# Kernel optimization log

Hardware: AMD Instinct MI355X
Metric: run time of the kernel (lower is better)

Reference implementation:

```python
import jax, jax.numpy as jnp
import numpy as np

H = 128        # hidden_dim
FEAT = 32      # feat_dim
LAYERS = 4     # 'layers' init arg -> residual MLP stacks of LAYERS+1 linears
M = 32768      # nodes per topological level
L = 16         # number of topological levels
MU = M // 2    # unary nodes per level (rest binary)
N = M * L      # total nodes


def setup_inputs() -> dict:
    key = jax.random.key(0)
    ks = jax.random.split(key, 10)

    def lin(k, out, inn):
        kw, kb = jax.random.split(k)
        s = 1.0 / np.sqrt(inn)
        return (jax.random.uniform(kw, (out, inn), minval=-s, maxval=s, dtype=jnp.float32),
                jax.random.uniform(kb, (out,), minval=-s, maxval=s, dtype=jnp.float32))

    def lin_stack(k, n, out, inn):
        kw, kb = jax.random.split(k)
        s = 1.0 / np.sqrt(inn)
        return (jax.random.uniform(kw, (n, out, inn), minval=-s, maxval=s, dtype=jnp.float32),
                jax.random.uniform(kb, (n, out), minval=-s, maxval=s, dtype=jnp.float32))

    emb_w, emb_b = lin(ks[0], H, FEAT)          # embed_op: feat_dim -> H
    ne0_w, ne0_b = lin(ks[1], H, 2 * H)         # node_embeds[0]: 2H -> H
    ne_w, ne_b = lin_stack(ks[2], LAYERS, H, H) # node_embeds[1..]: H -> H
    mpu_w, mpu_b = lin_stack(ks[3], LAYERS + 1, H, H)  # mp_unary: all H -> H
    mpb0_w, mpb0_b = lin(ks[4], H, 2 * H)       # mp_binary[0]: 2H -> H
    mpb_w, mpb_b = lin_stack(ks[5], LAYERS, H, H)      # mp_binary[1..]: H -> H

    node_feats = jax.random.normal(ks[6], (N, FEAT), dtype=jnp.float32)

    # Layered DAG: node at level l>=1 has two candidate parents in level l-1.
    pk = jax.random.split(ks[7], L)
    rows = [jnp.zeros((M, 2), dtype=jnp.int32)]  # level-0 rows unused
    for l in range(1, L):
        rows.append(jax.random.randint(pk[l], (M, 2), 0, M, dtype=jnp.int32) + (l - 1) * M)
    parents = jnp.concatenate(rows, 0)

    return dict(node_feats=node_feats, emb_w=emb_w, emb_b=emb_b,
                ne0_w=ne0_w, ne0_b=ne0_b, ne_w=ne_w, ne_b=ne_b,
                mpu_w=mpu_w, mpu_b=mpu_b, mpb0_w=mpb0_w, mpb0_b=mpb0_b,
                mpb_w=mpb_w, mpb_b=mpb_b, parents=parents)


def _stack_mlp(x, w0, b0, ws, bs):
    """relu(lay0) -> relu(lay1) -> residual relu layers: act(lay(a[-2]+a[-1]))."""
    a0 = jax.nn.relu(x @ w0.T + b0)
    a1 = jax.nn.relu(a0 @ ws[0].T + bs[0])
    p2, p1 = a0, a1
    for i in range(1, ws.shape[0]):
        cur = jax.nn.relu((p2 + p1) @ ws[i].T + bs[i])
        p2, p1 = p1, cur
    return p1


def reference(node_feats, emb_w, emb_b, ne0_w, ne0_b, ne_w, ne_b,
              mpu_w, mpu_b, mpb0_w, mpb0_b, mpb_w, mpb_b, parents):
    base = jax.nn.relu(node_feats @ emb_w.T + emb_b)  # [N, H] embed_op for all nodes
    E = jnp.zeros((N, H), dtype=base.dtype)
    E = E.at[:M].set(base[:M])  # roots: no messages -> embeds = relu(embed_op)
    for l in range(1, L):  # topological propagation, one level at a time
        s = l * M
        pl = parents[s:s + M]
        # unary nodes: gather one parent embedding, mp_unary stack
        msg_u = E[pl[:MU, 0]]                                  # [MU, H]
        redux_u = _stack_mlp(msg_u, mpu_w[0], mpu_b[0], mpu_w[1:], mpu_b[1:])
        # binary nodes: gather + concat two parent embeddings, mp_binary stack
        msg_b = E[pl[MU:]].reshape(M - MU, 2 * H)              # [MB, 2H]
        redux_b = _stack_mlp(msg_b, mpb0_w, mpb0_b, mpb_w, mpb_b)
        redux = jnp.concatenate([redux_u, redux_b], axis=0)    # [M, H]
        # apply_func: concat(embed, msgs_redux) -> node_embeds stack
        x = jnp.concatenate([base[s:s + M], redux], axis=-1)   # [M, 2H]
        E = E.at[s:s + M].set(_stack_mlp(x, ne0_w, ne0_b, ne_w, ne_b))
    return E
```

## Files before the change

kernel.cpp:

```cpp
#include <hip/hip_runtime.h>
#include <hip/hip_bf16.h>


#define H        128
#define FEAT     32
#define M_NODES  32768
#define L_LAYERS 16
#define MU_      (M_NODES / 2)
#define N_TOTAL  (M_NODES * L_LAYERS)

typedef __bf16 bf16x8 __attribute__((ext_vector_type(8)));
typedef __bf16 bf16x4 __attribute__((ext_vector_type(4)));
typedef float  f32x4  __attribute__((ext_vector_type(4)));

#define SLOT_MPU(l) ((l) * 32)
#define SLOT_MPB0   160
#define SLOT_MPB(l) (224 + (l) * 32)
#define SLOT_NE0    352
#define SLOT_NE(l)  (416 + (l) * 32)
#define TOTAL_FP    544

#define CG_SWZ(row, cg) ((cg) ^ ((row) & 7))

__global__ void prep_kernel(__bf16* __restrict__ frags,
                            const float* __restrict__ mpu_w,
                            const float* __restrict__ mpb0_w,
                            const float* __restrict__ mpb_w,
                            const float* __restrict__ ne0_w,
                            const float* __restrict__ ne_w) {
  int fp = blockIdx.x * 4 + (threadIdx.x >> 6);
  if (fp >= TOTAL_FP) return;
  int lane = threadIdx.x & 63;
  const float* src; int K; int idx;
  if (fp < 160)      { src = mpu_w + (fp >> 5) * H * H;         K = H;     idx = fp & 31; }
  else if (fp < 224) { src = mpb0_w;                            K = 2 * H; idx = fp - 160; }
  else if (fp < 352) { src = mpb_w + ((fp - 224) >> 5) * H * H; K = H;     idx = (fp - 224) & 31; }
  else if (fp < 416) { src = ne0_w;                             K = 2 * H; idx = fp - 352; }
  else               { src = ne_w + ((fp - 416) >> 5) * H * H;  K = H;     idx = (fp - 416) & 31; }
  int KT = K >> 5;
  int ct = idx / KT, kt = idx - ct * KT;
  int col = ct * 16 + (lane & 15);
  int k0  = kt * 32 + (lane >> 4) * 8;
  __bf16* dhi = frags + ((size_t)fp << 10) + lane * 8;
#pragma unroll
  for (int j = 0; j < 8; ++j) {
    float x  = src[col * K + k0 + j];
    __bf16 h = (__bf16)x;
    dhi[j]       = h;
    dhi[512 + j] = (__bf16)(x - (float)h);
  }
}

__global__ void embed_kernel(float* __restrict__ E,
                             const float* __restrict__ feats,
                             const float* __restrict__ emb_w,
                             const float* __restrict__ emb_b) {
  __shared__ float fl[64][36];
  int tid = threadIdx.x;
  size_t rbase = (size_t)blockIdx.x * 64;
  {
    int idx = tid;
#pragma unroll
    for (int rep = 0; rep < 2; ++rep, idx += 256) {
      int r = idx >> 3, c4 = idx & 7;
      *(f32x4*)&fl[r][c4 * 4] = *(const f32x4*)(feats + (rbase + r) * FEAT + c4 * 4);
    }
  }
  __syncthreads();
  int o = tid & 127, rh = tid >> 7;
  float w[32];
#pragma unroll
  for (int i = 0; i < 8; ++i) {
    f32x4 v = *(const f32x4*)(emb_w + o * FEAT + i * 4);
    w[i * 4 + 0] = v[0]; w[i * 4 + 1] = v[1]; w[i * 4 + 2] = v[2]; w[i * 4 + 3] = v[3];
  }
  float b = emb_b[o];
  for (int i = 0; i < 32; ++i) {
    int r = rh * 32 + i;
    float acc = b;
#pragma unroll
    for (int k4 = 0; k4 < 8; ++k4) {
      f32x4 f = *(const f32x4*)&fl[r][k4 * 4];
      acc += f[0] * w[k4 * 4] + f[1] * w[k4 * 4 + 1] + f[2] * w[k4 * 4 + 2] + f[3] * w[k4 * 4 + 3];
    }
    E[(rbase + r) * H + o] = fmaxf(acc, 0.f);
  }
}

struct Wkt { bf16x8 h[4]; bf16x8 l[4]; };

__device__ __forceinline__ void load_wkt(Wkt& w, const __bf16* __restrict__ frags,
                                         int slot, int KT, int kt, int wc, int lane) {
#pragma unroll
  for (int c = 0; c < 4; ++c) {
    const __bf16* fb =
        frags + (((size_t)(slot + (wc * 4 + c) * KT + kt)) << 10) + lane * 8;
    w.h[c] = *(const bf16x8*)fb;
    w.l[c] = *(const bf16x8*)(fb + 512);
  }
}

__device__ __forceinline__ void zero_acc(f32x4 (&acc)[2][4]) {
  f32x4 z = {0.f, 0.f, 0.f, 0.f};
#pragma unroll
  for (int i = 0; i < 2; ++i)
#pragma unroll
    for (int c = 0; c < 4; ++c) acc[i][c] = z;
}

__device__ __forceinline__ void gemm(f32x4 (&acc)[2][4],
                                     const __bf16* Ph, const __bf16* Pl,
                                     const __bf16* __restrict__ frags, int slot, int KT,
                                     int ktoff, int wr, int wc, int lane) {
  int r16 = lane & 15, g = lane >> 4;
  Wkt w0, w1;
  load_wkt(w0, frags, slot, KT, ktoff, wc, lane);
  bf16x8 ah[2][4], al[2][4];
#pragma unroll
  for (int i = 0; i < 2; ++i) {
    int row = wr * 32 + i * 16 + r16;
#pragma unroll
    for (int kt = 0; kt < 4; ++kt) {
      int off = row * H + CG_SWZ(row, kt * 4 + g) * 8;
      ah[i][kt] = *(const bf16x8*)(Ph + off);
      al[i][kt] = *(const bf16x8*)(Pl + off);
    }
  }
#pragma unroll
  for (int kt = 0; kt < 4; ++kt) {
    Wkt& cur = (kt & 1) ? w1 : w0;
    Wkt& nxt = (kt & 1) ? w0 : w1;
    if (kt < 3) load_wkt(nxt, frags, slot, KT, ktoff + kt + 1, wc, lane);
#pragma unroll
    for (int i = 0; i < 2; ++i)
#pragma unroll
      for (int c = 0; c < 4; ++c)
        acc[i][c] = __builtin_amdgcn_mfma_f32_16x16x32_bf16(cur.h[c], ah[i][kt], acc[i][c], 0, 0, 0);
#pragma unroll
    for (int i = 0; i < 2; ++i)
#pragma unroll
      for (int c = 0; c < 4; ++c)
        acc[i][c] = __builtin_amdgcn_mfma_f32_16x16x32_bf16(cur.l[c], ah[i][kt], acc[i][c], 0, 0, 0);
#pragma unroll
    for (int i = 0; i < 2; ++i)
#pragma unroll
      for (int c = 0; c < 4; ++c)
        acc[i][c] = __builtin_amdgcn_mfma_f32_16x16x32_bf16(cur.h[c], al[i][kt], acc[i][c], 0, 0, 0);
  }
}

__device__ __forceinline__ void epilogue(const f32x4 (&acc)[2][4], const float* __restrict__ bias,
                                         int mode, float* __restrict__ eout, int wr, int wc,
                                         int lane, __bf16* Ch, __bf16* Cl, __bf16* Sh, __bf16* Sl) {
  int r16 = lane & 15, g = lane >> 4;
#pragma unroll
  for (int c = 0; c < 4; ++c) {
    int c0 = wc * 64 + c * 16 + g * 4;
    f32x4 bv = *(const f32x4*)(bias + c0);
#pragma unroll
    for (int i = 0; i < 2; ++i) {
      int row = wr * 32 + i * 16 + r16;
      f32x4 v;
#pragma unroll
      for (int j = 0; j < 4; ++j) v[j] = fmaxf(acc[i][c][j] + bv[j], 0.f);
      if (mode == 2) {
        *(f32x4*)(eout + (size_t)row * H + c0) = v;
      } else {
        int off = row * H + CG_SWZ(row, c0 >> 3) * 8 + (c0 & 7);
        if (mode == 1) {
          bf16x4 oh = *(bf16x4*)(Ch + off), ol = *(bf16x4*)(Cl + off);
          bf16x4 sh, sl;
#pragma unroll
          for (int j = 0; j < 4; ++j) {
            float sv = v[j] + (float)oh[j] + (float)ol[j];
            __bf16 t = (__bf16)sv;
            sh[j] = t; sl[j] = (__bf16)(sv - (float)t);
          }
          *(bf16x4*)(Sh + off) = sh; *(bf16x4*)(Sl + off) = sl;
        }
        bf16x4 h, l;
#pragma unroll
        for (int j = 0; j < 4; ++j) {
          __bf16 t = (__bf16)v[j];
          h[j] = t; l[j] = (__bf16)(v[j] - (float)t);
        }
        *(bf16x4*)(Ch + off) = h; *(bf16x4*)(Cl + off) = l;
      }
    }
  }
}

__device__ __forceinline__ void stage_row(const float* __restrict__ src, __bf16* Ph, __bf16* Pl,
                                          int row, int q) {
#pragma unroll
  for (int i = 0; i < 4; ++i) {
    int cg = q * 4 + i;
    f32x4 f0 = *(const f32x4*)(src + cg * 8);
    f32x4 f1 = *(const f32x4*)(src + cg * 8 + 4);
    bf16x8 h, l;
#pragma unroll
    for (int j = 0; j < 4; ++j) {
      __bf16 t = (__bf16)f0[j]; h[j] = t; l[j] = (__bf16)(f0[j] - (float)t);
    }
#pragma unroll
    for (int j = 0; j < 4; ++j) {
      __bf16 t = (__bf16)f1[j]; h[4 + j] = t; l[4 + j] = (__bf16)(f1[j] - (float)t);
    }
    int off = row * H + CG_SWZ(row, cg) * 8;
    *(bf16x8*)(Ph + off) = h;
    *(bf16x8*)(Pl + off) = l;
  }
}

__global__ __launch_bounds__(256, 2) void phase_kernel(
    float* __restrict__ E, const int* __restrict__ parents, const __bf16* __restrict__ frags,
    const float* __restrict__ mpu_b, const float* __restrict__ mpb0_b,
    const float* __restrict__ mpb_b, const float* __restrict__ ne0_b,
    const float* __restrict__ ne_b, int s) {
  __shared__ __bf16 Ch[64 * H], Cl[64 * H], Sh[64 * H], Sl[64 * H];
  int t = blockIdx.x;
  bool un = t < (MU_ / 64);
  int row0 = t * 64;
  int tid = threadIdx.x;
  int lane = tid & 63, wave = tid >> 6;
  int wr = wave >> 1, wc = wave & 1;
  int srow = tid >> 2, q = tid & 3;
  int gr = s + row0 + srow;

  f32x4 acc[2][4];

  if (un) {
    stage_row(E + (size_t)parents[2 * gr] * H, Ch, Cl, srow, q);
    __syncthreads();
    zero_acc(acc); gemm(acc, Ch, Cl, frags, SLOT_MPU(0), 4, 0, wr, wc, lane); __syncthreads();
    epilogue(acc, mpu_b, 0, nullptr, wr, wc, lane, Ch, Cl, Sh, Sl); __syncthreads();
    zero_acc(acc); gemm(acc, Ch, Cl, frags, SLOT_MPU(1), 4, 0, wr, wc, lane); __syncthreads();
    epilogue(acc, mpu_b + H, 1, nullptr, wr, wc, lane, Ch, Cl, Sh, Sl); __syncthreads();
    zero_acc(acc); gemm(acc, Sh, Sl, frags, SLOT_MPU(2), 4, 0, wr, wc, lane); __syncthreads();
    epilogue(acc, mpu_b + 2 * H, 1, nullptr, wr, wc, lane, Ch, Cl, Sh, Sl); __syncthreads();
    zero_acc(acc); gemm(acc, Sh, Sl, frags, SLOT_MPU(3), 4, 0, wr, wc, lane); __syncthreads();
    epilogue(acc, mpu_b + 3 * H, 1, nullptr, wr, wc, lane, Ch, Cl, Sh, Sl); __syncthreads();
    zero_acc(acc); gemm(acc, Sh, Sl, frags, SLOT_MPU(4), 4, 0, wr, wc, lane); __syncthreads();
    epilogue(acc, mpu_b + 4 * H, 0, nullptr, wr, wc, lane, Ch, Cl, Sh, Sl);
  } else {
    stage_row(E + (size_t)parents[2 * gr] * H, Sh, Sl, srow, q);
    stage_row(E + (size_t)parents[2 * gr + 1] * H, Ch, Cl, srow, q);
    __syncthreads();
    zero_acc(acc);
    gemm(acc, Sh, Sl, frags, SLOT_MPB0, 8, 0, wr, wc, lane);
    gemm(acc, Ch, Cl, frags, SLOT_MPB0, 8, 4, wr, wc, lane);
    __syncthreads();
    epilogue(acc, mpb0_b, 0, nullptr, wr, wc, lane, Ch, Cl, Sh, Sl); __syncthreads();
    zero_acc(acc); gemm(acc, Ch, Cl, frags, SLOT_MPB(0), 4, 0, wr, wc, lane); __syncthreads();
    epilogue(acc, mpb_b, 1, nullptr, wr, wc, lane, Ch, Cl, Sh, Sl); __syncthreads();
    zero_acc(acc); gemm(acc, Sh, Sl, frags, SLOT_MPB(1), 4, 0, wr, wc, lane); __syncthreads();
    epilogue(acc, mpb_b + H, 1, nullptr, wr, wc, lane, Ch, Cl, Sh, Sl); __syncthreads();
    zero_acc(acc); gemm(acc, Sh, Sl, frags, SLOT_MPB(2), 4, 0, wr, wc, lane); __syncthreads();
    epilogue(acc, mpb_b + 2 * H, 1, nullptr, wr, wc, lane, Ch, Cl, Sh, Sl); __syncthreads();
    zero_acc(acc); gemm(acc, Sh, Sl, frags, SLOT_MPB(3), 4, 0, wr, wc, lane); __syncthreads();
    epilogue(acc, mpb_b + 3 * H, 0, nullptr, wr, wc, lane, Ch, Cl, Sh, Sl);
  }

  stage_row(E + (size_t)(s + row0 + srow) * H, Sh, Sl, srow, q);
  __syncthreads();

  zero_acc(acc);
  gemm(acc, Sh, Sl, frags, SLOT_NE0, 8, 0, wr, wc, lane);
  gemm(acc, Ch, Cl, frags, SLOT_NE0, 8, 4, wr, wc, lane);
  __syncthreads();
  epilogue(acc, ne0_b, 0, nullptr, wr, wc, lane, Ch, Cl, Sh, Sl); __syncthreads();
  zero_acc(acc); gemm(acc, Ch, Cl, frags, SLOT_NE(0), 4, 0, wr, wc, lane); __syncthreads();
  epilogue(acc, ne_b, 1, nullptr, wr, wc, lane, Ch, Cl, Sh, Sl); __syncthreads();
  zero_acc(acc); gemm(acc, Sh, Sl, frags, SLOT_NE(1), 4, 0, wr, wc, lane); __syncthreads();
  epilogue(acc, ne_b + H, 1, nullptr, wr, wc, lane, Ch, Cl, Sh, Sl); __syncthreads();
  zero_acc(acc); gemm(acc, Sh, Sl, frags, SLOT_NE(2), 4, 0, wr, wc, lane); __syncthreads();
  epilogue(acc, ne_b + 2 * H, 1, nullptr, wr, wc, lane, Ch, Cl, Sh, Sl); __syncthreads();
  zero_acc(acc); gemm(acc, Sh, Sl, frags, SLOT_NE(3), 4, 0, wr, wc, lane);
  epilogue(acc, ne_b + 3 * H, 2, E + (size_t)(s + row0) * H, wr, wc, lane, Ch, Cl, Sh, Sl);
}

extern "C" void kernel_launch(void* const* d_in, const int* in_sizes, int n_in,
                              void* d_out, int out_size, void* d_ws, size_t ws_size,
                              hipStream_t stream) {
  const float* node_feats = (const float*)d_in[0];
  const float* emb_w  = (const float*)d_in[1];
  const float* emb_b  = (const float*)d_in[2];
  const float* ne0_w  = (const float*)d_in[3];
  const float* ne0_b  = (const float*)d_in[4];
  const float* ne_w   = (const float*)d_in[5];
  const float* ne_b   = (const float*)d_in[6];
  const float* mpu_w  = (const float*)d_in[7];
  const float* mpu_b  = (const float*)d_in[8];
  const float* mpb0_w = (const float*)d_in[9];
  const float* mpb0_b = (const float*)d_in[10];
  const float* mpb_w  = (const float*)d_in[11];
  const float* mpb_b  = (const float*)d_in[12];
  const int*   parents = (const int*)d_in[13];
  float* E = (float*)d_out;
  __bf16* frags = (__bf16*)d_ws;

  prep_kernel<<<(TOTAL_FP + 3) / 4, 256, 0, stream>>>(frags, mpu_w, mpb0_w, mpb_w, ne0_w, ne_w);
  embed_kernel<<<N_TOTAL / 64, 256, 0, stream>>>(E, node_feats, emb_w, emb_b);
  for (int l = 1; l < L_LAYERS; ++l) {
    phase_kernel<<<M_NODES / 64, 256, 0, stream>>>(E, parents, frags, mpu_b, mpb0_b, mpb_b,
                                                   ne0_b, ne_b, l * M_NODES);
  }
}
```

Before: 1.160 ms.

## Keep MLP activations in registers per wave and fuse embed into phase kernel

Restructures the phase kernel so each wave owns 32 rows and feeds each layer's output accumulators straight into the next layer's MFMA input fragments in registers. This removes the shared-memory staging and the block-wide barriers between layers. The prep kernel now permutes the K ordering of the weight fragments so accumulator layout matches input fragment layout. The residual term is kept in per-wave shared scratch without syncs. The base embedding is computed on the fly with MFMA inside each phase rather than by a separate full-graph embed kernel, and only level 0 is embedded up front. In exchange, register pressure is higher, occupancy drops to one block per SM (launch bounds), and weight fragments are loaded from global memory more often.

```diff
diff --git a/kernel.cpp b/kernel.cpp
--- a/kernel.cpp
+++ b/kernel.cpp
@@ -7,22 +7,22 @@
 #define M_NODES  32768
 #define L_LAYERS 16
 #define MU_      (M_NODES / 2)
-#define N_TOTAL  (M_NODES * L_LAYERS)
 
 typedef __bf16 bf16x8 __attribute__((ext_vector_type(8)));
-typedef __bf16 bf16x4 __attribute__((ext_vector_type(4)));
 typedef float  f32x4  __attribute__((ext_vector_type(4)));
 
-#define SLOT_MPU(l) ((l) * 32)
-#define SLOT_MPB0   160
-#define SLOT_MPB(l) (224 + (l) * 32)
-#define SLOT_NE0    352
-#define SLOT_NE(l)  (416 + (l) * 32)
-#define TOTAL_FP    544
-
-#define CG_SWZ(row, cg) ((cg) ^ ((row) & 7))
+#define MFMA_BF16 __builtin_amdgcn_mfma_f32_16x16x32_bf16
+
+#define SLOT_EMB    0
+#define SLOT_MPU(l) (8 + (l) * 32)
+#define SLOT_MPB0   168
+#define SLOT_MPB(l) (232 + (l) * 32)
+#define SLOT_NE0    360
+#define SLOT_NE(l)  (424 + (l) * 32)
+#define TOTAL_FP    552
 
 __global__ void prep_kernel(__bf16* __restrict__ frags,
+                            const float* __restrict__ emb_w,
                             const float* __restrict__ mpu_w,
                             const float* __restrict__ mpb0_w,
                             const float* __restrict__ mpb_w,
@@ -31,252 +31,261 @@
   int fp = blockIdx.x * 4 + (threadIdx.x >> 6);
   if (fp >= TOTAL_FP) return;
   int lane = threadIdx.x & 63;
+  int r16 = lane & 15, g = lane >> 4;
   const float* src; int K; int idx;
-  if (fp < 160)      { src = mpu_w + (fp >> 5) * H * H;         K = H;     idx = fp & 31; }
-  else if (fp < 224) { src = mpb0_w;                            K = 2 * H; idx = fp - 160; }
-  else if (fp < 352) { src = mpb_w + ((fp - 224) >> 5) * H * H; K = H;     idx = (fp - 224) & 31; }
-  else if (fp < 416) { src = ne0_w;                             K = 2 * H; idx = fp - 352; }
-  else               { src = ne_w + ((fp - 416) >> 5) * H * H;  K = H;     idx = (fp - 416) & 31; }
+  if (fp < 8)        { src = emb_w;                             K = 32;  idx = fp; }
+  else if (fp < 168) { src = mpu_w + ((fp - 8) >> 5) * H * H;   K = 128; idx = (fp - 8) & 31; }
+  else if (fp < 232) { src = mpb0_w;                            K = 256; idx = fp - 168; }
+  else if (fp < 360) { src = mpb_w + ((fp - 232) >> 5) * H * H; K = 128; idx = (fp - 232) & 31; }
+  else if (fp < 424) { src = ne0_w;                             K = 256; idx = fp - 360; }
+  else               { src = ne_w + ((fp - 424) >> 5) * H * H;  K = 128; idx = (fp - 424) & 31; }
   int KT = K >> 5;
-  int ct = idx / KT, kt = idx - ct * KT;
-  int col = ct * 16 + (lane & 15);
-  int k0  = kt * 32 + (lane >> 4) * 8;
+  int c = idx / KT, kt = idx - c * KT;
+  int col = c * 16 + r16;
   __bf16* dhi = frags + ((size_t)fp << 10) + lane * 8;
 #pragma unroll
   for (int j = 0; j < 8; ++j) {
-    float x  = src[col * K + k0 + j];
+    int k = kt * 32 + ((j >> 2) * 16 + g * 4 + (j & 3));
+    float x  = src[col * K + k];
     __bf16 h = (__bf16)x;
     dhi[j]       = h;
     dhi[512 + j] = (__bf16)(x - (float)h);
   }
 }
 
-__global__ void embed_kernel(float* __restrict__ E,
-                             const float* __restrict__ feats,
-                             const float* __restrict__ emb_w,
-                             const float* __restrict__ emb_b) {
-  __shared__ float fl[64][36];
-  int tid = threadIdx.x;
-  size_t rbase = (size_t)blockIdx.x * 64;
-  {
-    int idx = tid;
-#pragma unroll
-    for (int rep = 0; rep < 2; ++rep, idx += 256) {
-      int r = idx >> 3, c4 = idx & 7;
-      *(f32x4*)&fl[r][c4 * 4] = *(const f32x4*)(feats + (rbase + r) * FEAT + c4 * 4);
-    }
-  }
-  __syncthreads();
-  int o = tid & 127, rh = tid >> 7;
-  float w[32];
-#pragma unroll
-  for (int i = 0; i < 8; ++i) {
-    f32x4 v = *(const f32x4*)(emb_w + o * FEAT + i * 4);
-    w[i * 4 + 0] = v[0]; w[i * 4 + 1] = v[1]; w[i * 4 + 2] = v[2]; w[i * 4 + 3] = v[3];
-  }
-  float b = emb_b[o];
-  for (int i = 0; i < 32; ++i) {
-    int r = rh * 32 + i;
-    float acc = b;
-#pragma unroll
-    for (int k4 = 0; k4 < 8; ++k4) {
-      f32x4 f = *(const f32x4*)&fl[r][k4 * 4];
-      acc += f[0] * w[k4 * 4] + f[1] * w[k4 * 4 + 1] + f[2] * w[k4 * 4 + 2] + f[3] * w[k4 * 4 + 3];
-    }
-    E[(rbase + r) * H + o] = fmaxf(acc, 0.f);
-  }
-}
-
-struct Wkt { bf16x8 h[4]; bf16x8 l[4]; };
-
-__device__ __forceinline__ void load_wkt(Wkt& w, const __bf16* __restrict__ frags,
-                                         int slot, int KT, int kt, int wc, int lane) {
-#pragma unroll
-  for (int c = 0; c < 4; ++c) {
-    const __bf16* fb =
-        frags + (((size_t)(slot + (wc * 4 + c) * KT + kt)) << 10) + lane * 8;
-    w.h[c] = *(const bf16x8*)fb;
-    w.l[c] = *(const bf16x8*)(fb + 512);
-  }
-}
-
-__device__ __forceinline__ void zero_acc(f32x4 (&acc)[2][4]) {
+__device__ __forceinline__ void split_pair(const f32x4& a, const f32x4& b,
+                                           bf16x8& h, bf16x8& l) {
+#pragma unroll
+  for (int j = 0; j < 4; ++j) {
+    __bf16 t = (__bf16)a[j]; h[j] = t;     l[j] = (__bf16)(a[j] - (float)t);
+    __bf16 u = (__bf16)b[j]; h[4 + j] = u; l[4 + j] = (__bf16)(b[j] - (float)u);
+  }
+}
+
+__device__ __forceinline__ void zero_acc8(f32x4 (&acc)[2][8]) {
   f32x4 z = {0.f, 0.f, 0.f, 0.f};
 #pragma unroll
   for (int i = 0; i < 2; ++i)
 #pragma unroll
-    for (int c = 0; c < 4; ++c) acc[i][c] = z;
-}
-
-__device__ __forceinline__ void gemm(f32x4 (&acc)[2][4],
-                                     const __bf16* Ph, const __bf16* Pl,
-                                     const __bf16* __restrict__ frags, int slot, int KT,
-                                     int ktoff, int wr, int wc, int lane) {
+    for (int c = 0; c < 8; ++c) acc[i][c] = z;
+}
+
+__device__ __forceinline__ void gather_frags128(bf16x8 (&xh)[2][4], bf16x8 (&xl)[2][4],
+                                                const float* __restrict__ s0,
+                                                const float* __restrict__ s1, int g) {
+#pragma unroll
+  for (int i = 0; i < 2; ++i) {
+    const float* src = i ? s1 : s0;
+#pragma unroll
+    for (int kt = 0; kt < 4; ++kt) {
+      f32x4 a = *(const f32x4*)(src + kt * 32 + g * 4);
+      f32x4 b = *(const f32x4*)(src + kt * 32 + 16 + g * 4);
+      split_pair(a, b, xh[i][kt], xl[i][kt]);
+    }
+  }
+}
+
+__device__ __forceinline__ void stage128(f32x4 (&acc)[2][8],
+                                         const bf16x8 (&xh)[2][4], const bf16x8 (&xl)[2][4],
+                                         const __bf16* __restrict__ frags,
+                                         int fp0, int KT, int kt0, int lane) {
+#pragma unroll
+  for (int cp = 0; cp < 4; ++cp) {
+    const int c0 = 2 * cp, c1 = 2 * cp + 1;
+#pragma unroll
+    for (int kt = 0; kt < 4; ++kt) {
+      const __bf16* f0 = frags + (((size_t)(fp0 + c0 * KT + kt0 + kt)) << 10) + lane * 8;
+      const __bf16* f1 = frags + (((size_t)(fp0 + c1 * KT + kt0 + kt)) << 10) + lane * 8;
+      bf16x8 w0h = *(const bf16x8*)f0;
+      bf16x8 w0l = *(const bf16x8*)(f0 + 512);
+      bf16x8 w1h = *(const bf16x8*)f1;
+      bf16x8 w1l = *(const bf16x8*)(f1 + 512);
+      acc[0][c0] = MFMA_BF16(w0h, xh[0][kt], acc[0][c0], 0, 0, 0);
+      acc[0][c1] = MFMA_BF16(w1h, xh[0][kt], acc[0][c1], 0, 0, 0);
+      acc[1][c0] = MFMA_BF16(w0h, xh[1][kt], acc[1][c0], 0, 0, 0);
+      acc[1][c1] = MFMA_BF16(w1h, xh[1][kt], acc[1][c1], 0, 0, 0);
+      acc[0][c0] = MFMA_BF16(w0l, xh[0][kt], acc[0][c0], 0, 0, 0);
+      acc[0][c1] = MFMA_BF16(w1l, xh[0][kt], acc[0][c1], 0, 0, 0);
+      acc[1][c0] = MFMA_BF16(w0l, xh[1][kt], acc[1][c0], 0, 0, 0);
+      acc[1][c1] = MFMA_BF16(w1l, xh[1][kt], acc[1][c1], 0, 0, 0);
+      acc[0][c0] = MFMA_BF16(w0h, xl[0][kt], acc[0][c0], 0, 0, 0);
+      acc[0][c1] = MFMA_BF16(w1h, xl[0][kt], acc[0][c1], 0, 0, 0);
+      acc[1][c0] = MFMA_BF16(w0h, xl[1][kt], acc[1][c0], 0, 0, 0);
+      acc[1][c1] = MFMA_BF16(w1h, xl[1][kt], acc[1][c1], 0, 0, 0);
+    }
+  }
+}
+
+__device__ __forceinline__ void stage32(f32x4 (&acc)[2][8],
+                                        const bf16x8 (&fh)[2], const bf16x8 (&fl)[2],
+                                        const __bf16* __restrict__ frags, int fp0, int lane) {
+#pragma unroll
+  for (int cp = 0; cp < 4; ++cp) {
+    const int c0 = 2 * cp, c1 = 2 * cp + 1;
+    const __bf16* f0 = frags + (((size_t)(fp0 + c0)) << 10) + lane * 8;
+    const __bf16* f1 = frags + (((size_t)(fp0 + c1)) << 10) + lane * 8;
+    bf16x8 w0h = *(const bf16x8*)f0;
+    bf16x8 w0l = *(const bf16x8*)(f0 + 512);
+    bf16x8 w1h = *(const bf16x8*)f1;
+    bf16x8 w1l = *(const bf16x8*)(f1 + 512);
+    acc[0][c0] = MFMA_BF16(w0h, fh[0], acc[0][c0], 0, 0, 0);
+    acc[0][c1] = MFMA_BF16(w1h, fh[0], acc[0][c1], 0, 0, 0);
+    acc[1][c0] = MFMA_BF16(w0h, fh[1], acc[1][c0], 0, 0, 0);
+    acc[1][c1] = MFMA_BF16(w1h, fh[1], acc[1][c1], 0, 0, 0);
+    acc[0][c0] = MFMA_BF16(w0l, fh[0], acc[0][c0], 0, 0, 0);
+    acc[0][c1] = MFMA_BF16(w1l, fh[0], acc[0][c1], 0, 0, 0);
+    acc[1][c0] = MFMA_BF16(w0l, fh[1], acc[1][c0], 0, 0, 0);
+    acc[1][c1] = MFMA_BF16(w1l, fh[1], acc[1][c1], 0, 0, 0);
+    acc[0][c0] = MFMA_BF16(w0h, fl[0], acc[0][c0], 0, 0, 0);
+    acc[0][c1] = MFMA_BF16(w1h, fl[0], acc[0][c1], 0, 0, 0);
+    acc[1][c0] = MFMA_BF16(w0h, fl[1], acc[1][c0], 0, 0, 0);
+    acc[1][c1] = MFMA_BF16(w1h, fl[1], acc[1][c1], 0, 0, 0);
+  }
+}
+
+template <int PM>
+__device__ __forceinline__ void epilogue_frags(const f32x4 (&acc)[2][8],
+                                               const float* __restrict__ bias,
+                                               float* pv, int g,
+                                               bf16x8 (&xh)[2][4], bf16x8 (&xl)[2][4]) {
+#pragma unroll
+  for (int i = 0; i < 2; ++i)
+#pragma unroll
+    for (int kt = 0; kt < 4; ++kt) {
+      f32x4 x0, x1;
+#pragma unroll
+      for (int hf = 0; hf < 2; ++hf) {
+        const int c = 2 * kt + hf;
+        f32x4 bv = *(const f32x4*)(bias + c * 16 + g * 4);
+        f32x4 a, x;
+#pragma unroll
+        for (int j = 0; j < 4; ++j) a[j] = fmaxf(acc[i][c][j] + bv[j], 0.f);
+        x = a;
+        if (PM == 1) {
+          f32x4 p = *(const f32x4*)(pv + (i * 8 + c) * 256);
+#pragma unroll
+          for (int j = 0; j < 4; ++j) x[j] = a[j] + p[j];
+        }
+        if (PM != 2) *(f32x4*)(pv + (i * 8 + c) * 256) = a;
+        if (hf == 0) x0 = x; else x1 = x;
+      }
+      split_pair(x0, x1, xh[i][kt], xl[i][kt]);
+    }
+}
+
+__device__ __forceinline__ void epilogue_store(const f32x4 (&acc)[2][8],
+                                               const float* __restrict__ bias,
+                                               float* __restrict__ out, int r16, int g) {
+#pragma unroll
+  for (int i = 0; i < 2; ++i)
+#pragma unroll
+    for (int c = 0; c < 8; ++c) {
+      f32x4 bv = *(const f32x4*)(bias + c * 16 + g * 4);
+      f32x4 v;
+#pragma unroll
+      for (int j = 0; j < 4; ++j) v[j] = fmaxf(acc[i][c][j] + bv[j], 0.f);
+      *(f32x4*)(out + (size_t)(i * 16 + r16) * H + c * 16 + g * 4) = v;
+    }
+}
+
+__device__ __forceinline__ void feats_frags(bf16x8 (&fh)[2], bf16x8 (&fl)[2],
+                                            const float* __restrict__ feats,
+                                            int row_a, int row_b, int g) {
+#pragma unroll
+  for (int i = 0; i < 2; ++i) {
+    const float* src = feats + (size_t)(i ? row_b : row_a) * FEAT;
+    f32x4 a = *(const f32x4*)(src + g * 4);
+    f32x4 b = *(const f32x4*)(src + 16 + g * 4);
+    split_pair(a, b, fh[i], fl[i]);
+  }
+}
+
+__global__ __launch_bounds__(256, 1) void base0_kernel(float* __restrict__ E,
+                                                       const float* __restrict__ feats,
+                                                       const __bf16* __restrict__ frags,
+                                                       const float* __restrict__ emb_b) {
+  int tid = threadIdx.x, lane = tid & 63, wave = tid >> 6;
   int r16 = lane & 15, g = lane >> 4;
-  Wkt w0, w1;
-  load_wkt(w0, frags, slot, KT, ktoff, wc, lane);
-  bf16x8 ah[2][4], al[2][4];
-#pragma unroll
-  for (int i = 0; i < 2; ++i) {
-    int row = wr * 32 + i * 16 + r16;
-#pragma unroll
-    for (int kt = 0; kt < 4; ++kt) {
-      int off = row * H + CG_SWZ(row, kt * 4 + g) * 8;
-      ah[i][kt] = *(const bf16x8*)(Ph + off);
-      al[i][kt] = *(const bf16x8*)(Pl + off);
-    }
-  }
-#pragma unroll
-  for (int kt = 0; kt < 4; ++kt) {
-    Wkt& cur = (kt & 1) ? w1 : w0;
-    Wkt& nxt = (kt & 1) ? w0 : w1;
-    if (kt < 3) load_wkt(nxt, frags, slot, KT, ktoff + kt + 1, wc, lane);
-#pragma unroll
-    for (int i = 0; i < 2; ++i)
-#pragma unroll
-      for (int c = 0; c < 4; ++c)
-        acc[i][c] = __builtin_amdgcn_mfma_f32_16x16x32_bf16(cur.h[c], ah[i][kt], acc[i][c], 0, 0, 0);
-#pragma unroll
-    for (int i = 0; i < 2; ++i)
-#pragma unroll
-      for (int c = 0; c < 4; ++c)
-        acc[i][c] = __builtin_amdgcn_mfma_f32_16x16x32_bf16(cur.l[c], ah[i][kt], acc[i][c], 0, 0, 0);
-#pragma unroll
-    for (int i = 0; i < 2; ++i)
-#pragma unroll
-      for (int c = 0; c < 4; ++c)
-        acc[i][c] = __builtin_amdgcn_mfma_f32_16x16x32_bf16(cur.h[c], al[i][kt], acc[i][c], 0, 0, 0);
-  }
-}
-
-__device__ __forceinline__ void epilogue(const f32x4 (&acc)[2][4], const float* __restrict__ bias,
-                                         int mode, float* __restrict__ eout, int wr, int wc,
-                                         int lane, __bf16* Ch, __bf16* Cl, __bf16* Sh, __bf16* Sl) {
-  int r16 = lane & 15, g = lane >> 4;
-#pragma unroll
-  for (int c = 0; c < 4; ++c) {
-    int c0 = wc * 64 + c * 16 + g * 4;
-    f32x4 bv = *(const f32x4*)(bias + c0);
-#pragma unroll
-    for (int i = 0; i < 2; ++i) {
-      int row = wr * 32 + i * 16 + r16;
-      f32x4 v;
-#pragma unroll
-      for (int j = 0; j < 4; ++j) v[j] = fmaxf(acc[i][c][j] + bv[j], 0.f);
-      if (mode == 2) {
-        *(f32x4*)(eout + (size_t)row * H + c0) = v;
-      } else {
-        int off = row * H + CG_SWZ(row, c0 >> 3) * 8 + (c0 & 7);
-        if (mode == 1) {
-          bf16x4 oh = *(bf16x4*)(Ch + off), ol = *(bf16x4*)(Cl + off);
-          bf16x4 sh, sl;
-#pragma unroll
-          for (int j = 0; j < 4; ++j) {
-            float sv = v[j] + (float)oh[j] + (float)ol[j];
-            __bf16 t = (__bf16)sv;
-            sh[j] = t; sl[j] = (__bf16)(sv - (float)t);
-          }
-          *(bf16x4*)(Sh + off) = sh; *(bf16x4*)(Sl + off) = sl;
-        }
-        bf16x4 h, l;
-#pragma unroll
-        for (int j = 0; j < 4; ++j) {
-          __bf16 t = (__bf16)v[j];
-          h[j] = t; l[j] = (__bf16)(v[j] - (float)t);
-        }
-        *(bf16x4*)(Ch + off) = h; *(bf16x4*)(Cl + off) = l;
-      }
-    }
-  }
-}
-
-__device__ __forceinline__ void stage_row(const float* __restrict__ src, __bf16* Ph, __bf16* Pl,
-                                          int row, int q) {
-#pragma unroll
-  for (int i = 0; i < 4; ++i) {
-    int cg = q * 4 + i;
-    f32x4 f0 = *(const f32x4*)(src + cg * 8);
-    f32x4 f1 = *(const f32x4*)(src + cg * 8 + 4);
-    bf16x8 h, l;
-#pragma unroll
-    for (int j = 0; j < 4; ++j) {
-      __bf16 t = (__bf16)f0[j]; h[j] = t; l[j] = (__bf16)(f0[j] - (float)t);
-    }
-#pragma unroll
-    for (int j = 0; j < 4; ++j) {
-      __bf16 t = (__bf16)f1[j]; h[4 + j] = t; l[4 + j] = (__bf16)(f1[j] - (float)t);
-    }
-    int off = row * H + CG_SWZ(row, cg) * 8;
-    *(bf16x8*)(Ph + off) = h;
-    *(bf16x8*)(Pl + off) = l;
-  }
-}
-
-__global__ __launch_bounds__(256, 2) void phase_kernel(
-    float* __restrict__ E, const int* __restrict__ parents, const __bf16* __restrict__ frags,
+  int R0 = blockIdx.x * 128 + wave * 32;
+  bf16x8 fh[2], fl[2];
+  feats_frags(fh, fl, feats, R0 + r16, R0 + 16 + r16, g);
+  f32x4 acc[2][8];
+  zero_acc8(acc);
+  stage32(acc, fh, fl, frags, SLOT_EMB, lane);
+  epilogue_store(acc, emb_b, E + (size_t)R0 * H, r16, g);
+}
+
+__global__ __launch_bounds__(256, 1) void phase_kernel(
+    float* __restrict__ E, const int* __restrict__ parents,
+    const __bf16* __restrict__ frags, const float* __restrict__ feats,
+    const float* __restrict__ emb_b,
     const float* __restrict__ mpu_b, const float* __restrict__ mpb0_b,
     const float* __restrict__ mpb_b, const float* __restrict__ ne0_b,
     const float* __restrict__ ne_b, int s) {
-  __shared__ __bf16 Ch[64 * H], Cl[64 * H], Sh[64 * H], Sl[64 * H];
-  int t = blockIdx.x;
-  bool un = t < (MU_ / 64);
-  int row0 = t * 64;
-  int tid = threadIdx.x;
-  int lane = tid & 63, wave = tid >> 6;
-  int wr = wave >> 1, wc = wave & 1;
-  int srow = tid >> 2, q = tid & 3;
-  int gr = s + row0 + srow;
-
-  f32x4 acc[2][4];
-
-  if (un) {
-    stage_row(E + (size_t)parents[2 * gr] * H, Ch, Cl, srow, q);
-    __syncthreads();
-    zero_acc(acc); gemm(acc, Ch, Cl, frags, SLOT_MPU(0), 4, 0, wr, wc, lane); __syncthreads();
-    epilogue(acc, mpu_b, 0, nullptr, wr, wc, lane, Ch, Cl, Sh, Sl); __syncthreads();
-    zero_acc(acc); gemm(acc, Ch, Cl, frags, SLOT_MPU(1), 4, 0, wr, wc, lane); __syncthreads();
-    epilogue(acc, mpu_b + H, 1, nullptr, wr, wc, lane, Ch, Cl, Sh, Sl); __syncthreads();
-    zero_acc(acc); gemm(acc, Sh, Sl, frags, SLOT_MPU(2), 4, 0, wr, wc, lane); __syncthreads();
-    epilogue(acc, mpu_b + 2 * H, 1, nullptr, wr, wc, lane, Ch, Cl, Sh, Sl); __syncthreads();
-    zero_acc(acc); gemm(acc, Sh, Sl, frags, SLOT_MPU(3), 4, 0, wr, wc, lane); __syncthreads();
-    epilogue(acc, mpu_b + 3 * H, 1, nullptr, wr, wc, lane, Ch, Cl, Sh, Sl); __syncthreads();
-    zero_acc(acc); gemm(acc, Sh, Sl, frags, SLOT_MPU(4), 4, 0, wr, wc, lane); __syncthreads();
-    epilogue(acc, mpu_b + 4 * H, 0, nullptr, wr, wc, lane, Ch, Cl, Sh, Sl);
+  __shared__ float prevb[4 * 4096];
+  int tid = threadIdx.x, lane = tid & 63, wave = tid >> 6;
+  int r16 = lane & 15, g = lane >> 4;
+  int R0 = blockIdx.x * 128 + wave * 32;
+  float* pv = prevb + wave * 4096 + lane * 4;
+  int gr_a = s + R0 + r16;
+  int gr_b = gr_a + 16;
+
+  f32x4 acc[2][8];
+  bf16x8 xh[2][4], xl[2][4];
+
+  if (R0 < MU_) {
+    int pa = parents[2 * gr_a], pb = parents[2 * gr_b];
+    gather_frags128(xh, xl, E + (size_t)pa * H, E + (size_t)pb * H, g);
+    zero_acc8(acc);
+    stage128(acc, xh, xl, frags, SLOT_MPU(0), 4, 0, lane);
+    epilogue_frags<0>(acc, mpu_b, pv, g, xh, xl);
+    for (int l = 1; l <= 3; ++l) {
+      zero_acc8(acc);
+      stage128(acc, xh, xl, frags, SLOT_MPU(l), 4, 0, lane);
+      epilogue_frags<1>(acc, mpu_b + l * H, pv, g, xh, xl);
+    }
+    zero_acc8(acc);
+    stage128(acc, xh, xl, frags, SLOT_MPU(4), 4, 0, lane);
+    epilogue_frags<2>(acc, mpu_b + 4 * H, pv, g, xh, xl);
   } else {
-    stage_row(E + (size_t)parents[2 * gr] * H, Sh, Sl, srow, q);
-    stage_row(E + (size_t)parents[2 * gr + 1] * H, Ch, Cl, srow, q);
-    __syncthreads();
-    zero_acc(acc);
-    gemm(acc, Sh, Sl, frags, SLOT_MPB0, 8, 0, wr, wc, lane);
-    gemm(acc, Ch, Cl, frags, SLOT_MPB0, 8, 4, wr, wc, lane);
-    __syncthreads();
-    epilogue(acc, mpb0_b, 0, nullptr, wr, wc, lane, Ch, Cl, Sh, Sl); __syncthreads();
-    zero_acc(acc); gemm(acc, Ch, Cl, frags, SLOT_MPB(0), 4, 0, wr, wc, lane); __syncthreads();
-    epilogue(acc, mpb_b, 1, nullptr, wr, wc, lane, Ch, Cl, Sh, Sl); __syncthreads();
-    zero_acc(acc); gemm(acc, Sh, Sl, frags, SLOT_MPB(1), 4, 0, wr, wc, lane); __syncthreads();
-    epilogue(acc, mpb_b + H, 1, nullptr, wr, wc, lane, Ch, Cl, Sh, Sl); __syncthreads();
-    zero_acc(acc); gemm(acc, Sh, Sl, frags, SLOT_MPB(2), 4, 0, wr, wc, lane); __syncthreads();
-    epilogue(acc, mpb_b + 2 * H, 1, nullptr, wr, wc, lane, Ch, Cl, Sh, Sl); __syncthreads();
-    zero_acc(acc); gemm(acc, Sh, Sl, frags, SLOT_MPB(3), 4, 0, wr, wc, lane); __syncthreads();
-    epilogue(acc, mpb_b + 3 * H, 0, nullptr, wr, wc, lane, Ch, Cl, Sh, Sl);
-  }
-
-  stage_row(E + (size_t)(s + row0 + srow) * H, Sh, Sl, srow, q);
-  __syncthreads();
-
-  zero_acc(acc);
-  gemm(acc, Sh, Sl, frags, SLOT_NE0, 8, 0, wr, wc, lane);
-  gemm(acc, Ch, Cl, frags, SLOT_NE0, 8, 4, wr, wc, lane);
-  __syncthreads();
-  epilogue(acc, ne0_b, 0, nullptr, wr, wc, lane, Ch, Cl, Sh, Sl); __syncthreads();
-  zero_acc(acc); gemm(acc, Ch, Cl, frags, SLOT_NE(0), 4, 0, wr, wc, lane); __syncthreads();
-  epilogue(acc, ne_b, 1, nullptr, wr, wc, lane, Ch, Cl, Sh, Sl); __syncthreads();
-  zero_acc(acc); gemm(acc, Sh, Sl, frags, SLOT_NE(1), 4, 0, wr, wc, lane); __syncthreads();
-  epilogue(acc, ne_b + H, 1, nullptr, wr, wc, lane, Ch, Cl, Sh, Sl); __syncthreads();
-  zero_acc(acc); gemm(acc, Sh, Sl, frags, SLOT_NE(2), 4, 0, wr, wc, lane); __syncthreads();
-  epilogue(acc, ne_b + 2 * H, 1, nullptr, wr, wc, lane, Ch, Cl, Sh, Sl); __syncthreads();
-  zero_acc(acc); gemm(acc, Sh, Sl, frags, SLOT_NE(3), 4, 0, wr, wc, lane);
-  epilogue(acc, ne_b + 3 * H, 2, E + (size_t)(s + row0) * H, wr, wc, lane, Ch, Cl, Sh, Sl);
+    int p0a = parents[2 * gr_a], p1a = parents[2 * gr_a + 1];
+    int p0b = parents[2 * gr_b], p1b = parents[2 * gr_b + 1];
+    gather_frags128(xh, xl, E + (size_t)p0a * H, E + (size_t)p0b * H, g);
+    zero_acc8(acc);
+    stage128(acc, xh, xl, frags, SLOT_MPB0, 8, 0, lane);
+    gather_frags128(xh, xl, E + (size_t)p1a * H, E + (size_t)p1b * H, g);
+    stage128(acc, xh, xl, frags, SLOT_MPB0, 8, 4, lane);
+    epilogue_frags<0>(acc, mpb0_b, pv, g, xh, xl);
+    for (int l = 0; l <= 2; ++l) {
+      zero_acc8(acc);
+      stage128(acc, xh, xl, frags, SLOT_MPB(l), 4, 0, lane);
+      epilogue_frags<1>(acc, mpb_b + l * H, pv, g, xh, xl);
+    }
+    zero_acc8(acc);
+    stage128(acc, xh, xl, frags, SLOT_MPB(3), 4, 0, lane);
+    epilogue_frags<2>(acc, mpb_b + 3 * H, pv, g, xh, xl);
+  }
+
+  zero_acc8(acc);
+  stage128(acc, xh, xl, frags, SLOT_NE0, 8, 4, lane);
+  {
+    bf16x8 fh[2], fl[2];
+    feats_frags(fh, fl, feats, gr_a, gr_b, g);
+    f32x4 acc2[2][8];
+    zero_acc8(acc2);
+    stage32(acc2, fh, fl, frags, SLOT_EMB, lane);
+    epilogue_frags<2>(acc2, emb_b, pv, g, xh, xl);
+  }
+  stage128(acc, xh, xl, frags, SLOT_NE0, 8, 0, lane);
+  epilogue_frags<0>(acc, ne0_b, pv, g, xh, xl);
+  for (int l = 0; l <= 2; ++l) {
+    zero_acc8(acc);
+    stage128(acc, xh, xl, frags, SLOT_NE(l), 4, 0, lane);
+    epilogue_frags<1>(acc, ne_b + l * H, pv, g, xh, xl);
+  }
+  zero_acc8(acc);
+  stage128(acc, xh, xl, frags, SLOT_NE(3), 4, 0, lane);
+  epilogue_store(acc, ne_b + 3 * H, E + (size_t)(s + R0) * H, r16, g);
 }
 
 extern "C" void kernel_launch(void* const* d_in, const int* in_sizes, int n_in,
@@ -299,10 +308,12 @@
   float* E = (float*)d_out;
   __bf16* frags = (__bf16*)d_ws;
 
-  prep_kernel<<<(TOTAL_FP + 3) / 4, 256, 0, stream>>>(frags, mpu_w, mpb0_w, mpb_w, ne0_w, ne_w);
-  embed_kernel<<<N_TOTAL / 64, 256, 0, stream>>>(E, node_feats, emb_w, emb_b);
+  prep_kernel<<<(TOTAL_FP + 3) / 4, 256, 0, stream>>>(frags, emb_w, mpu_w, mpb0_w,
+                                                      mpb_w, ne0_w, ne_w);
+  base0_kernel<<<M_NODES / 128, 256, 0, stream>>>(E, node_feats, frags, emb_b);
   for (int l = 1; l < L_LAYERS; ++l) {
-    phase_kernel<<<M_NODES / 64, 256, 0, stream>>>(E, parents, frags, mpu_b, mpb0_b, mpb_b,
-                                                   ne0_b, ne_b, l * M_NODES);
-  }
-}
+    phase_kernel<<<M_NODES / 128, 256, 0, stream>>>(E, parents, frags, node_feats,
+                                                    emb_b, mpu_b, mpb0_b, mpb_b,
+                                                    ne0_b, ne_b, l * M_NODES);
+  }
+}
```

New measurement: 1.358 ms. +17.1%, slower.
